# Optimization experiments

Hardware: AMD Instinct MI355X
Metric: run time of the kernel (lower is better)

The kernel has to match this reference:

```python
import jax, jax.numpy as jnp
import numpy as np


def setup_inputs() -> dict:
    key = jax.random.key(0)
    k1, k2 = jax.random.split(key)
    B, T, D = 16, 4096, 512
    x = jax.random.normal(k1, (B, T, D), dtype=jnp.float32)
    alpha = jax.random.normal(k2, (1, 1, D), dtype=jnp.float32)  # raw param, pre-sigmoid
    return {"x": x, "alpha": alpha}


def reference(x, alpha):
    # s_0 = x_0 ; s_t = a * x_t + (1 - a) * s_{t-1}, a = sigmoid(alpha)
    a = jax.nn.sigmoid(alpha[0, 0, :])  # (D,)
    one_minus_a = 1.0 - a

    def step(prev, xt):  # prev, xt: (B, D)
        cur = a * xt + one_minus_a * prev
        return cur, cur

    x_t = jnp.swapaxes(x, 0, 1)  # (T, B, D)
    init = x_t[0]
    _, rest = jax.lax.scan(step, init, x_t[1:])  # (T-1, B, D)
    states = jnp.concatenate([x_t[:1], rest], axis=0)  # (T, B, D)
    return jnp.swapaxes(states, 0, 1)  # (B, T, D)
```

## Files before the change

### kernel.cpp

```cpp
#include <hip/hip_runtime.h>
#include <math.h>

#define BB 16
#define TT 4096
#define DD 512
#define D4 128

typedef float v4f __attribute__((ext_vector_type(4)));

__device__ __forceinline__ float sigmf(float v) {
    return 1.0f / (1.0f + expf(-v));
}

__device__ __forceinline__ void nt_store4(float4* p, const float4& s) {
    __builtin_nontemporal_store(*reinterpret_cast<const v4f*>(&s),
                                reinterpret_cast<v4f*>(p));
}

__global__ __launch_bounds__(256) void es_chunk_ends(
    const float* __restrict__ x, const float* __restrict__ alpha,
    float* __restrict__ ends, int C, int L)
{
    const int c   = blockIdx.x;
    const int tid = threadIdx.x;
    const int b   = (blockIdx.y << 1) + (tid >> 7);
    const int d4  = tid & 127;

    const float4 al = reinterpret_cast<const float4*>(alpha)[d4];
    const float ax = sigmf(al.x), ay = sigmf(al.y), az = sigmf(al.z), aw = sigmf(al.w);
    const float fx = 1.0f - ax, fy = 1.0f - ay, fz = 1.0f - az, fw = 1.0f - aw;

    const float4* xp = reinterpret_cast<const float4*>(x)
                     + ((size_t)b * TT + (size_t)c * L) * D4 + d4;

    float4 s;
    if (c == 0) {
        s = xp[0];
    } else {
        s.x = s.y = s.z = s.w = 0.0f;
    }

    #pragma unroll 8
    for (int i = 0; i < L; ++i) {
        const float4 v = xp[(size_t)i * D4];
        s.x = fmaf(ax, v.x, fx * s.x);
        s.y = fmaf(ay, v.y, fy * s.y);
        s.z = fmaf(az, v.z, fz * s.z);
        s.w = fmaf(aw, v.w, fw * s.w);
    }

    reinterpret_cast<float4*>(ends)[((size_t)b * C + c) * D4 + d4] = s;
}

__global__ __launch_bounds__(256) void es_final_fused(
    const float* __restrict__ x, const float* __restrict__ alpha,
    const float* __restrict__ ends, float* __restrict__ out, int C, int L)
{
    const int c   = blockIdx.x;
    const int tid = threadIdx.x;
    const int b   = (blockIdx.y << 1) + (tid >> 7);
    const int d4  = tid & 127;

    const float4 al = reinterpret_cast<const float4*>(alpha)[d4];
    const float ax = sigmf(al.x), ay = sigmf(al.y), az = sigmf(al.z), aw = sigmf(al.w);
    const float fx = 1.0f - ax, fy = 1.0f - ay, fz = 1.0f - az, fw = 1.0f - aw;

    const size_t base = ((size_t)b * TT + (size_t)c * L) * D4 + d4;
    const float4* xp = reinterpret_cast<const float4*>(x) + base;
    float4*       op = reinterpret_cast<float4*>(out) + base;

    float4 s;
    if (c == 0) {
        s = xp[0];
    } else {
        float4 fL;
        fL.x = powf(fx, (float)L);
        fL.y = powf(fy, (float)L);
        fL.z = powf(fz, (float)L);
        fL.w = powf(fw, (float)L);

        const float4* e = reinterpret_cast<const float4*>(ends)
                        + (size_t)b * C * D4 + d4;

        float4 S = e[0];
        int j = 1;
        for (; j + 8 <= c; j += 8) {
            float4 v[8];
            #pragma unroll
            for (int k = 0; k < 8; ++k) v[k] = e[(size_t)(j + k) * D4];
            #pragma unroll
            for (int k = 0; k < 8; ++k) {
                S.x = fmaf(fL.x, S.x, v[k].x);
                S.y = fmaf(fL.y, S.y, v[k].y);
                S.z = fmaf(fL.z, S.z, v[k].z);
                S.w = fmaf(fL.w, S.w, v[k].w);
            }
        }
        for (; j < c; ++j) {
            const float4 v = e[(size_t)j * D4];
            S.x = fmaf(fL.x, S.x, v.x);
            S.y = fmaf(fL.y, S.y, v.y);
            S.z = fmaf(fL.z, S.z, v.z);
            S.w = fmaf(fL.w, S.w, v.w);
        }
        s = S;
    }

    #pragma unroll 8
    for (int i = 0; i < L; ++i) {
        const float4 v = xp[(size_t)i * D4];
        s.x = fmaf(ax, v.x, fx * s.x);
        s.y = fmaf(ay, v.y, fy * s.y);
        s.z = fmaf(az, v.z, fz * s.z);
        s.w = fmaf(aw, v.w, fw * s.w);
        nt_store4(op + (size_t)i * D4, s);
    }
}

__global__ __launch_bounds__(256) void es_serial(
    const float* __restrict__ x, const float* __restrict__ alpha,
    float* __restrict__ out)
{
    const int g  = blockIdx.x * 256 + threadIdx.x;
    const int b  = g >> 7;
    const int d4 = g & 127;

    const float4 al = reinterpret_cast<const float4*>(alpha)[d4];
    const float ax = sigmf(al.x), ay = sigmf(al.y), az = sigmf(al.z), aw = sigmf(al.w);
    const float fx = 1.0f - ax, fy = 1.0f - ay, fz = 1.0f - az, fw = 1.0f - aw;

    const float4* xp = reinterpret_cast<const float4*>(x) + (size_t)b * TT * D4 + d4;
    float4*       op = reinterpret_cast<float4*>(out) + (size_t)b * TT * D4 + d4;

    float4 s = xp[0];
    #pragma unroll 4
    for (int t = 0; t < TT; ++t) {
        const float4 v = xp[(size_t)t * D4];
        s.x = fmaf(ax, v.x, fx * s.x);
        s.y = fmaf(ay, v.y, fy * s.y);
        s.z = fmaf(az, v.z, fz * s.z);
        s.w = fmaf(aw, v.w, fw * s.w);
        op[(size_t)t * D4] = s;
    }
}

extern "C" void kernel_launch(void* const* d_in, const int* in_sizes, int n_in,
                              void* d_out, int out_size, void* d_ws, size_t ws_size,
                              hipStream_t stream)
{
    const float* x     = (const float*)d_in[0];
    const float* alpha = (const float*)d_in[1];
    float*       out   = (float*)d_out;

    int C = 128;
    while (C > 8 && (size_t)BB * C * DD * sizeof(float) > ws_size) C >>= 1;

    if ((size_t)BB * C * DD * sizeof(float) > ws_size) {
        es_serial<<<dim3(8), 256, 0, stream>>>(x, alpha, out);
        return;
    }

    const int L = TT / C;
    float* ends = (float*)d_ws;

    es_chunk_ends<<<dim3(C, BB / 2), 256, 0, stream>>>(x, alpha, ends, C, L);
    es_final_fused<<<dim3(C, BB / 2), 256, 0, stream>>>(x, alpha, ends, out, C, L);
}
```

Baseline: 261.5 us.

## Fuse chunk scan into single kernel with ticketed decoupled lookback

```diff
diff --git a/kernel.cpp b/kernel.cpp
--- a/kernel.cpp
+++ b/kernel.cpp
@@ -5,6 +5,12 @@
 #define TT 4096
 #define DD 512
 #define D4 128
+#define CC 128
+#define LL 32
+#define NBY 8
+
+#define FLAGS_OFF_U32 64
+#define ENDS_OFF_B    8192
 
 typedef float v4f __attribute__((ext_vector_type(4)));
 
@@ -17,84 +23,88 @@
                                 reinterpret_cast<v4f*>(p));
 }
 
-__global__ __launch_bounds__(256) void es_chunk_ends(
+__global__ __launch_bounds__(256) void es_single(
     const float* __restrict__ x, const float* __restrict__ alpha,
-    float* __restrict__ ends, int C, int L)
+    unsigned int* __restrict__ hdr, float* __restrict__ out)
 {
-    const int c   = blockIdx.x;
     const int tid = threadIdx.x;
-    const int b   = (blockIdx.y << 1) + (tid >> 7);
-    const int d4  = tid & 127;
+
+    __shared__ unsigned int tkt_s;
+    if (tid == 0) tkt_s = atomicAdd(hdr, 1u);
+    __syncthreads();
+    const unsigned int t = tkt_s;
+    const int by = (int)(t & (NBY - 1));
+    const int c  = (int)(t >> 3);
+
+    const int b  = (by << 1) + (tid >> 7);
+    const int d4 = tid & 127;
+
+    unsigned int* flags = hdr + FLAGS_OFF_U32;
+    float4* ends = reinterpret_cast<float4*>(reinterpret_cast<char*>(hdr) + ENDS_OFF_B);
 
     const float4 al = reinterpret_cast<const float4*>(alpha)[d4];
     const float ax = sigmf(al.x), ay = sigmf(al.y), az = sigmf(al.z), aw = sigmf(al.w);
     const float fx = 1.0f - ax, fy = 1.0f - ay, fz = 1.0f - az, fw = 1.0f - aw;
 
-    const float4* xp = reinterpret_cast<const float4*>(x)
-                     + ((size_t)b * TT + (size_t)c * L) * D4 + d4;
-
-    float4 s;
-    if (c == 0) {
-        s = xp[0];
-    } else {
-        s.x = s.y = s.z = s.w = 0.0f;
-    }
-
-    #pragma unroll 8
-    for (int i = 0; i < L; ++i) {
-        const float4 v = xp[(size_t)i * D4];
-        s.x = fmaf(ax, v.x, fx * s.x);
-        s.y = fmaf(ay, v.y, fy * s.y);
-        s.z = fmaf(az, v.z, fz * s.z);
-        s.w = fmaf(aw, v.w, fw * s.w);
-    }
-
-    reinterpret_cast<float4*>(ends)[((size_t)b * C + c) * D4 + d4] = s;
-}
-
-__global__ __launch_bounds__(256) void es_final_fused(
-    const float* __restrict__ x, const float* __restrict__ alpha,
-    const float* __restrict__ ends, float* __restrict__ out, int C, int L)
-{
-    const int c   = blockIdx.x;
-    const int tid = threadIdx.x;
-    const int b   = (blockIdx.y << 1) + (tid >> 7);
-    const int d4  = tid & 127;
-
-    const float4 al = reinterpret_cast<const float4*>(alpha)[d4];
-    const float ax = sigmf(al.x), ay = sigmf(al.y), az = sigmf(al.z), aw = sigmf(al.w);
-    const float fx = 1.0f - ax, fy = 1.0f - ay, fz = 1.0f - az, fw = 1.0f - aw;
-
-    const size_t base = ((size_t)b * TT + (size_t)c * L) * D4 + d4;
+    const size_t base = ((size_t)b * TT + (size_t)c * LL) * D4 + d4;
     const float4* xp = reinterpret_cast<const float4*>(x) + base;
     float4*       op = reinterpret_cast<float4*>(out) + base;
 
+    float4 buf[LL];
+    #pragma unroll
+    for (int i = 0; i < LL; ++i) buf[i] = xp[(size_t)i * D4];
+
     float4 s;
-    if (c == 0) {
-        s = xp[0];
-    } else {
+    if (c == 0) { s = buf[0]; }
+    else        { s.x = s.y = s.z = s.w = 0.0f; }
+    #pragma unroll
+    for (int i = 0; i < LL; ++i) {
+        s.x = fmaf(ax, buf[i].x, fx * s.x);
+        s.y = fmaf(ay, buf[i].y, fy * s.y);
+        s.z = fmaf(az, buf[i].z, fz * s.z);
+        s.w = fmaf(aw, buf[i].w, fw * s.w);
+    }
+    ends[((size_t)b * CC + c) * D4 + d4] = s;
+
+    __syncthreads();
+    if (tid == 0) {
+        __hip_atomic_store(&flags[(by << 7) + c], 1u,
+                           __ATOMIC_RELEASE, __HIP_MEMORY_SCOPE_AGENT);
+    }
+
+    float4 S;
+    if (c > 0) {
+        if (tid < c) {
+            while (__hip_atomic_load(&flags[(by << 7) + tid],
+                                     __ATOMIC_RELAXED, __HIP_MEMORY_SCOPE_AGENT) == 0u) {
+                __builtin_amdgcn_s_sleep(2);
+            }
+        }
+        __syncthreads();
+        __builtin_amdgcn_fence(__ATOMIC_ACQUIRE, "agent");
+
         float4 fL;
-        fL.x = powf(fx, (float)L);
-        fL.y = powf(fy, (float)L);
-        fL.z = powf(fz, (float)L);
-        fL.w = powf(fw, (float)L);
+        fL.x = powf(fx, (float)LL);
+        fL.y = powf(fy, (float)LL);
+        fL.z = powf(fz, (float)LL);
+        fL.w = powf(fw, (float)LL);
 
-        const float4* e = reinterpret_cast<const float4*>(ends)
-                        + (size_t)b * C * D4 + d4;
-
-        float4 S = e[0];
+        const float4* e = ends + (size_t)b * CC * D4 + d4;
+        S = e[0];
         int j = 1;
-        for (; j + 8 <= c; j += 8) {
-            float4 v[8];
-            #pragma unroll
-            for (int k = 0; k < 8; ++k) v[k] = e[(size_t)(j + k) * D4];
-            #pragma unroll
-            for (int k = 0; k < 8; ++k) {
-                S.x = fmaf(fL.x, S.x, v[k].x);
-                S.y = fmaf(fL.y, S.y, v[k].y);
-                S.z = fmaf(fL.z, S.z, v[k].z);
-                S.w = fmaf(fL.w, S.w, v[k].w);
-            }
+        for (; j + 4 <= c; j += 4) {
+            float4 v0 = e[(size_t)(j + 0) * D4];
+            float4 v1 = e[(size_t)(j + 1) * D4];
+            float4 v2 = e[(size_t)(j + 2) * D4];
+            float4 v3 = e[(size_t)(j + 3) * D4];
+            S.x = fmaf(fL.x, S.x, v0.x); S.y = fmaf(fL.y, S.y, v0.y);
+            S.z = fmaf(fL.z, S.z, v0.z); S.w = fmaf(fL.w, S.w, v0.w);
+            S.x = fmaf(fL.x, S.x, v1.x); S.y = fmaf(fL.y, S.y, v1.y);
+            S.z = fmaf(fL.z, S.z, v1.z); S.w = fmaf(fL.w, S.w, v1.w);
+            S.x = fmaf(fL.x, S.x, v2.x); S.y = fmaf(fL.y, S.y, v2.y);
+            S.z = fmaf(fL.z, S.z, v2.z); S.w = fmaf(fL.w, S.w, v2.w);
+            S.x = fmaf(fL.x, S.x, v3.x); S.y = fmaf(fL.y, S.y, v3.y);
+            S.z = fmaf(fL.z, S.z, v3.z); S.w = fmaf(fL.w, S.w, v3.w);
         }
         for (; j < c; ++j) {
             const float4 v = e[(size_t)j * D4];
@@ -103,17 +113,18 @@
             S.z = fmaf(fL.z, S.z, v.z);
             S.w = fmaf(fL.w, S.w, v.w);
         }
-        s = S;
     }
 
-    #pragma unroll 8
-    for (int i = 0; i < L; ++i) {
-        const float4 v = xp[(size_t)i * D4];
-        s.x = fmaf(ax, v.x, fx * s.x);
-        s.y = fmaf(ay, v.y, fy * s.y);
-        s.z = fmaf(az, v.z, fz * s.z);
-        s.w = fmaf(aw, v.w, fw * s.w);
-        nt_store4(op + (size_t)i * D4, s);
+    float4 sf;
+    if (c == 0) sf = buf[0];
+    else        sf = S;
+    #pragma unroll
+    for (int i = 0; i < LL; ++i) {
+        sf.x = fmaf(ax, buf[i].x, fx * sf.x);
+        sf.y = fmaf(ay, buf[i].y, fy * sf.y);
+        sf.z = fmaf(az, buf[i].z, fz * sf.z);
+        sf.w = fmaf(aw, buf[i].w, fw * sf.w);
+        nt_store4(op + (size_t)i * D4, sf);
     }
 }
 
@@ -152,17 +163,14 @@
     const float* alpha = (const float*)d_in[1];
     float*       out   = (float*)d_out;
 
-    int C = 128;
-    while (C > 8 && (size_t)BB * C * DD * sizeof(float) > ws_size) C >>= 1;
-
-    if ((size_t)BB * C * DD * sizeof(float) > ws_size) {
+    const size_t need = (size_t)ENDS_OFF_B + (size_t)BB * CC * DD * sizeof(float);
+    if (ws_size < need) {
         es_serial<<<dim3(8), 256, 0, stream>>>(x, alpha, out);
         return;
     }
 
-    const int L = TT / C;
-    float* ends = (float*)d_ws;
+    hipMemsetAsync(d_ws, 0, ENDS_OFF_B, stream);
 
-    es_chunk_ends<<<dim3(C, BB / 2), 256, 0, stream>>>(x, alpha, ends, C, L);
-    es_final_fused<<<dim3(C, BB / 2), 256, 0, stream>>>(x, alpha, ends, out, C, L);
+    es_single<<<dim3(CC * NBY), 256, 0, stream>>>(
+        x, alpha, (unsigned int*)d_ws, out);
 }
```

After: 322.0 us. 23.1% more time.
